# Kernel optimization log

Hardware: AMD Instinct MI355X
Metric: run time of the kernel (lower is better)

The kernel has to match this reference:

```python
import jax, jax.numpy as jnp
import numpy as np

N_NODES = 40000
N_EDGES = 640000
D = 128
D_OUT = 128


def _layernorm(x, gamma, beta, eps=1e-5):
    mu = jnp.mean(x, axis=-1, keepdims=True)
    var = jnp.mean(jnp.square(x - mu), axis=-1, keepdims=True)
    return (x - mu) * jax.lax.rsqrt(var + eps) * gamma + beta


def setup_inputs() -> dict:
    key = jax.random.key(0)
    ks = jax.random.split(key, 6)
    x = jax.random.normal(ks[0], (N_NODES, D), dtype=jnp.float32)
    edge_index = jax.random.randint(ks[1], (2, N_EDGES), 0, N_NODES, dtype=jnp.int64)
    s = 1.0 / np.sqrt(D)
    return {
        "x": x,
        "edge_index": edge_index,
        "ln1_w": jnp.ones((D,), jnp.float32),
        "ln1_b": jnp.zeros((D,), jnp.float32),
        "ln2_w": jnp.ones((D,), jnp.float32),
        "ln2_b": jnp.zeros((D,), jnp.float32),
        "w": jnp.ones((D,), jnp.float32),
        "W1": jax.random.normal(ks[2], (D, D), jnp.float32) * s,
        "W2": jax.random.normal(ks[3], (D, D), jnp.float32) * s,
        "O1": jax.random.normal(ks[4], (2 * D, D), jnp.float32) * s,
        "O2": jax.random.normal(ks[5], (D, D_OUT), jnp.float32) * s,
    }


def reference(x, edge_index, ln1_w, ln1_b, ln2_w, ln2_b, w, W1, W2, O1, O2):
    row, col = edge_index[0], edge_index[1]
    n = x.shape[0]
    # gather + 2-layer message MLP (bias-free): [E, D]
    msg = jnp.maximum(x[row] @ W1, 0.0) @ W2
    # scatter_mean over destination nodes (zero where no incoming edges)
    agg = jax.ops.segment_sum(msg, col, num_segments=n)
    cnt = jax.ops.segment_sum(jnp.ones((msg.shape[0],), x.dtype), col, num_segments=n)
    agg = agg / jnp.maximum(cnt, 1.0)[:, None]
    agg_n = _layernorm(agg, ln1_w, ln1_b)
    # repulsion + residual + LayerNorm
    fx = _layernorm(x + (x - agg_n) * w, ln2_w, ln2_b)
    # concat + output MLP
    cat = jnp.concatenate([fx, agg_n], axis=1)
    return jnp.maximum(cat @ O1, 0.0) @ O2
```

## Files before the change

### kernel.cpp

```cpp
#include <hip/hip_runtime.h>
#include <hip/hip_bf16.h>

#define NN 40000
#define NE 640000
#define DD 128
#define CAP 64
#define SLICE 5000
#define FILLB 640
#define FCHUNK 8000

typedef __attribute__((ext_vector_type(8))) short bf16x8;
typedef __attribute__((ext_vector_type(8))) unsigned short u16x8;
typedef __attribute__((ext_vector_type(4))) float f32x4;

__device__ __forceinline__ unsigned short f2bf(float f) {
    __hip_bfloat16 h = __float2bfloat16(f);
    return *reinterpret_cast<unsigned short*>(&h);
}
__device__ __forceinline__ float bf2f(unsigned short u) {
    union { unsigned int ui; float f; } v;
    v.ui = ((unsigned int)u) << 16;
    return v.f;
}

__global__ __launch_bounds__(256) void prep_kernel(
    const float* __restrict__ W1, const float* __restrict__ W2,
    const float* __restrict__ O1, const float* __restrict__ O2,
    unsigned short* __restrict__ w1t, unsigned short* __restrict__ w2t,
    unsigned short* __restrict__ o1t, unsigned short* __restrict__ o2t,
    unsigned int* __restrict__ cnt)
{
    int bx = blockIdx.x;
    if (bx >= 320) {
        int t = (bx - 320) * 256 + threadIdx.x;
        if (t < NN) cnt[t] = 0u;
        return;
    }
    int t = bx * 256 + threadIdx.x;
    if (t < 16384) {
        int n = t >> 7, k = t & 127;
        w1t[t] = f2bf(W1[k * 128 + n]);
    } else if (t < 32768) {
        int i = t - 16384;
        int n = i >> 7, k = i & 127;
        w2t[i] = f2bf(W2[k * 128 + n]);
    } else if (t < 65536) {
        int i = t - 32768;
        int n = i >> 8, k = i & 255;
        o1t[i] = f2bf(O1[k * 128 + n]);
    } else {
        int i = t - 65536;
        int n = i >> 7, k = i & 127;
        o2t[i] = f2bf(O2[k * 128 + n]);
    }
}

__global__ __launch_bounds__(256) void mega1_kernel(
    const float* __restrict__ x, const unsigned short* __restrict__ w1t,
    const unsigned short* __restrict__ w2t, unsigned short* __restrict__ nm,
    const int* __restrict__ ei, unsigned int* __restrict__ cnt,
    unsigned short* __restrict__ srcs)
{
    __shared__ unsigned short xt[64 * 128];
    __shared__ unsigned short wb[128 * 128];
    const int tid = threadIdx.x;
    const int bx = blockIdx.x;

    if (bx >= 625) {
        const int fb = bx - 625;
        const int slice = bx & 7;
        const int rank = fb >> 3;
        const int base = rank * FCHUNK;
        for (int j = tid; j < FCHUNK; j += 256) {
            int e = base + j;
            int d = ei[NE + e];
            int s = ei[e];
            if ((unsigned)d / SLICE == (unsigned)slice) {
                unsigned int p = atomicAdd(cnt + d, 1u);
                if (p < CAP) srcs[(size_t)d * CAP + p] = (unsigned short)s;
            }
        }
        return;
    }

    const int row0 = bx * 64;

    #pragma unroll
    for (int it = 0; it < 4; ++it) {
        int c = tid + it * 256;
        int r = c >> 4;
        int c0 = (c & 15) << 3;
        const float4* gp = reinterpret_cast<const float4*>(x + (size_t)(row0 + r) * DD + c0);
        float4 f0 = gp[0], f1 = gp[1];
        u16x8 p;
        p[0] = f2bf(f0.x); p[1] = f2bf(f0.y); p[2] = f2bf(f0.z); p[3] = f2bf(f0.w);
        p[4] = f2bf(f1.x); p[5] = f2bf(f1.y); p[6] = f2bf(f1.z); p[7] = f2bf(f1.w);
        unsigned b = (unsigned)((r * DD + c0) * 2) ^ ((unsigned)(r & 7) << 4);
        *reinterpret_cast<u16x8*>(reinterpret_cast<char*>(xt) + b) = p;
    }
    #pragma unroll
    for (int it = 0; it < 8; ++it) {
        int c = tid + it * 256;
        int n = c >> 4;
        int k0 = (c & 15) << 3;
        u16x8 v = *reinterpret_cast<const u16x8*>(w1t + n * DD + k0);
        unsigned b = (unsigned)((n * DD + k0) * 2) ^ ((unsigned)(n & 7) << 4);
        *reinterpret_cast<u16x8*>(reinterpret_cast<char*>(wb) + b) = v;
    }
    __syncthreads();

    const int lane = tid & 63;
    const int wv = tid >> 6;
    const int l15 = lane & 15;
    const int lg = lane >> 4;

    f32x4 acc[8];
    #pragma unroll
    for (int i = 0; i < 8; ++i) acc[i] = (f32x4){0.f, 0.f, 0.f, 0.f};

    #pragma unroll
    for (int kk = 0; kk < 4; ++kk) {
        int k = kk * 32 + lg * 8;
        int ar = wv * 16 + l15;
        bf16x8 a = *reinterpret_cast<const bf16x8*>(
            reinterpret_cast<const char*>(xt) + ((unsigned)((ar * DD + k) * 2) ^ ((unsigned)(ar & 7) << 4)));
        #pragma unroll
        for (int n0 = 0; n0 < 8; ++n0) {
            int bn = n0 * 16 + l15;
            bf16x8 bf = *reinterpret_cast<const bf16x8*>(
                reinterpret_cast<const char*>(wb) + ((unsigned)((bn * DD + k) * 2) ^ ((unsigned)(bn & 7) << 4)));
            acc[n0] = __builtin_amdgcn_mfma_f32_16x16x32_bf16(a, bf, acc[n0], 0, 0, 0);
        }
    }
    __syncthreads();

    unsigned short* hb = xt;
    #pragma unroll
    for (int n0 = 0; n0 < 8; ++n0) {
        #pragma unroll
        for (int ri = 0; ri < 4; ++ri) {
            int r = wv * 16 + lg * 4 + ri;
            int cc = n0 * 16 + l15;
            float v = fmaxf(acc[n0][ri], 0.0f);
            *reinterpret_cast<unsigned short*>(
                reinterpret_cast<char*>(hb) + ((unsigned)((r * DD + cc) * 2) ^ ((unsigned)(r & 7) << 4))) = f2bf(v);
        }
    }
    #pragma unroll
    for (int it = 0; it < 8; ++it) {
        int c = tid + it * 256;
        int n = c >> 4;
        int k0 = (c & 15) << 3;
        u16x8 v = *reinterpret_cast<const u16x8*>(w2t + n * DD + k0);
        unsigned b = (unsigned)((n * DD + k0) * 2) ^ ((unsigned)(n & 7) << 4);
        *reinterpret_cast<u16x8*>(reinterpret_cast<char*>(wb) + b) = v;
    }
    __syncthreads();

    f32x4 acc2[8];
    #pragma unroll
    for (int i = 0; i < 8; ++i) acc2[i] = (f32x4){0.f, 0.f, 0.f, 0.f};
    #pragma unroll
    for (int kk = 0; kk < 4; ++kk) {
        int k = kk * 32 + lg * 8;
        int ar = wv * 16 + l15;
        bf16x8 a = *reinterpret_cast<const bf16x8*>(
            reinterpret_cast<const char*>(hb) + ((unsigned)((ar * DD + k) * 2) ^ ((unsigned)(ar & 7) << 4)));
        #pragma unroll
        for (int n0 = 0; n0 < 8; ++n0) {
            int bn = n0 * 16 + l15;
            bf16x8 bf = *reinterpret_cast<const bf16x8*>(
                reinterpret_cast<const char*>(wb) + ((unsigned)((bn * DD + k) * 2) ^ ((unsigned)(bn & 7) << 4)));
            acc2[n0] = __builtin_amdgcn_mfma_f32_16x16x32_bf16(a, bf, acc2[n0], 0, 0, 0);
        }
    }
    #pragma unroll
    for (int n0 = 0; n0 < 8; ++n0) {
        #pragma unroll
        for (int ri = 0; ri < 4; ++ri) {
            int r = row0 + wv * 16 + lg * 4 + ri;
            int cc = n0 * 16 + l15;
            nm[(size_t)r * DD + cc] = f2bf(acc2[n0][ri]);
        }
    }
}

__global__ __launch_bounds__(256) void pull_node_kernel(
    const unsigned short* __restrict__ nm, const unsigned short* __restrict__ srcs,
    const unsigned int* __restrict__ cnt,
    const float* __restrict__ x,
    const float* __restrict__ g1, const float* __restrict__ b1,
    const float* __restrict__ g2, const float* __restrict__ b2,
    const float* __restrict__ w, unsigned short* __restrict__ catb)
{
    const int lane = threadIdx.x & 63;
    const int wv = threadIdx.x >> 6;
    const int i = blockIdx.x * 4 + wv;
    const int d0 = lane * 2;

    const unsigned int degf = cnt[i];
    const int deg = (int)(degf < CAP ? degf : CAP);
    const unsigned short* sp = srcs + (size_t)i * CAP;

    float a0 = 0.f, a1 = 0.f;
    int e = 0;
    for (; e + 8 <= deg; e += 8) {
        int s[8];
        #pragma unroll
        for (int j = 0; j < 8; ++j) s[j] = sp[e + j];
        ushort2 m[8];
        #pragma unroll
        for (int j = 0; j < 8; ++j)
            m[j] = *reinterpret_cast<const ushort2*>(nm + (size_t)s[j] * DD + d0);
        #pragma unroll
        for (int j = 0; j < 8; ++j) { a0 += bf2f(m[j].x); a1 += bf2f(m[j].y); }
    }
    for (; e + 4 <= deg; e += 4) {
        int s0 = sp[e + 0], s1 = sp[e + 1], s2 = sp[e + 2], s3 = sp[e + 3];
        ushort2 m0 = *reinterpret_cast<const ushort2*>(nm + (size_t)s0 * DD + d0);
        ushort2 m1 = *reinterpret_cast<const ushort2*>(nm + (size_t)s1 * DD + d0);
        ushort2 m2 = *reinterpret_cast<const ushort2*>(nm + (size_t)s2 * DD + d0);
        ushort2 m3 = *reinterpret_cast<const ushort2*>(nm + (size_t)s3 * DD + d0);
        a0 += bf2f(m0.x) + bf2f(m1.x) + bf2f(m2.x) + bf2f(m3.x);
        a1 += bf2f(m0.y) + bf2f(m1.y) + bf2f(m2.y) + bf2f(m3.y);
    }
    for (; e < deg; ++e) {
        int s0 = sp[e];
        ushort2 m0 = *reinterpret_cast<const ushort2*>(nm + (size_t)s0 * DD + d0);
        a0 += bf2f(m0.x);
        a1 += bf2f(m0.y);
    }

    float inv = 1.0f / fmaxf((float)degf, 1.0f);
    a0 *= inv; a1 *= inv;

    float s = a0 + a1;
    #pragma unroll
    for (int o = 32; o > 0; o >>= 1) s += __shfl_xor(s, o, 64);
    float mu = s * (1.0f / 128.0f);
    float e0 = a0 - mu, e1 = a1 - mu;
    float q = e0 * e0 + e1 * e1;
    #pragma unroll
    for (int o = 32; o > 0; o >>= 1) q += __shfl_xor(q, o, 64);
    float rs = rsqrtf(q * (1.0f / 128.0f) + 1e-5f);

    float2 g1v = *reinterpret_cast<const float2*>(g1 + d0);
    float2 b1v = *reinterpret_cast<const float2*>(b1 + d0);
    float an0 = e0 * rs * g1v.x + b1v.x;
    float an1 = e1 * rs * g1v.y + b1v.y;

    float2 xv = *reinterpret_cast<const float2*>(x + (size_t)i * DD + d0);
    float2 wv2 = *reinterpret_cast<const float2*>(w + d0);
    float t0 = xv.x + (xv.x - an0) * wv2.x;
    float t1 = xv.y + (xv.y - an1) * wv2.y;

    float s2 = t0 + t1;
    #pragma unroll
    for (int o = 32; o > 0; o >>= 1) s2 += __shfl_xor(s2, o, 64);
    float mu2 = s2 * (1.0f / 128.0f);
    float f0 = t0 - mu2, f1 = t1 - mu2;
    float q2 = f0 * f0 + f1 * f1;
    #pragma unroll
    for (int o = 32; o > 0; o >>= 1) q2 += __shfl_xor(q2, o, 64);
    float rs2 = rsqrtf(q2 * (1.0f / 128.0f) + 1e-5f);

    float2 g2v = *reinterpret_cast<const float2*>(g2 + d0);
    float2 b2v = *reinterpret_cast<const float2*>(b2 + d0);
    float fx0 = f0 * rs2 * g2v.x + b2v.x;
    float fx1 = f1 * rs2 * g2v.y + b2v.y;

    ushort2 uo; uo.x = f2bf(fx0); uo.y = f2bf(fx1);
    *reinterpret_cast<ushort2*>(catb + (size_t)i * 256 + d0) = uo;
    ushort2 ua; ua.x = f2bf(an0); ua.y = f2bf(an1);
    *reinterpret_cast<ushort2*>(catb + (size_t)i * 256 + 128 + d0) = ua;
}

__global__ __launch_bounds__(256) void mlp2_kernel(
    const unsigned short* __restrict__ catb, const unsigned short* __restrict__ o1t,
    const unsigned short* __restrict__ o2t, float* __restrict__ out)
{
    __shared__ unsigned short ct[64 * 128];
    __shared__ unsigned short wb[128 * 128];
    const int tid = threadIdx.x;
    const int row0 = blockIdx.x * 64;
    const int lane = tid & 63;
    const int wv = tid >> 6;
    const int l15 = lane & 15;
    const int lg = lane >> 4;

    f32x4 acc[8];
    #pragma unroll
    for (int i = 0; i < 8; ++i) acc[i] = (f32x4){0.f, 0.f, 0.f, 0.f};

    for (int h = 0; h < 2; ++h) {
        #pragma unroll
        for (int it = 0; it < 4; ++it) {
            int c = tid + it * 256;
            int r = c >> 4;
            int c0 = (c & 15) << 3;
            u16x8 v = *reinterpret_cast<const u16x8*>(catb + (size_t)(row0 + r) * 256 + h * 128 + c0);
            unsigned b = (unsigned)((r * 128 + c0) * 2) ^ ((unsigned)(r & 7) << 4);
            *reinterpret_cast<u16x8*>(reinterpret_cast<char*>(ct) + b) = v;
        }
        #pragma unroll
        for (int it = 0; it < 8; ++it) {
            int c = tid + it * 256;
            int n = c >> 4;
            int k0 = (c & 15) << 3;
            u16x8 v = *reinterpret_cast<const u16x8*>(o1t + n * 256 + h * 128 + k0);
            unsigned b = (unsigned)((n * 128 + k0) * 2) ^ ((unsigned)(n & 7) << 4);
            *reinterpret_cast<u16x8*>(reinterpret_cast<char*>(wb) + b) = v;
        }
        __syncthreads();
        #pragma unroll
        for (int kk = 0; kk < 4; ++kk) {
            int k = kk * 32 + lg * 8;
            int ar = wv * 16 + l15;
            bf16x8 a = *reinterpret_cast<const bf16x8*>(
                reinterpret_cast<const char*>(ct) + ((unsigned)((ar * 128 + k) * 2) ^ ((unsigned)(ar & 7) << 4)));
            #pragma unroll
            for (int n0 = 0; n0 < 8; ++n0) {
                int bn = n0 * 16 + l15;
                bf16x8 bf = *reinterpret_cast<const bf16x8*>(
                    reinterpret_cast<const char*>(wb) + ((unsigned)((bn * 128 + k) * 2) ^ ((unsigned)(bn & 7) << 4)));
                acc[n0] = __builtin_amdgcn_mfma_f32_16x16x32_bf16(a, bf, acc[n0], 0, 0, 0);
            }
        }
        __syncthreads();
    }

    unsigned short* hb = ct;
    #pragma unroll
    for (int n0 = 0; n0 < 8; ++n0) {
        #pragma unroll
        for (int ri = 0; ri < 4; ++ri) {
            int r = wv * 16 + lg * 4 + ri;
            int cc = n0 * 16 + l15;
            float v = fmaxf(acc[n0][ri], 0.0f);
            *reinterpret_cast<unsigned short*>(
                reinterpret_cast<char*>(hb) + ((unsigned)((r * DD + cc) * 2) ^ ((unsigned)(r & 7) << 4))) = f2bf(v);
        }
    }
    #pragma unroll
    for (int it = 0; it < 8; ++it) {
        int c = tid + it * 256;
        int n = c >> 4;
        int k0 = (c & 15) << 3;
        u16x8 v = *reinterpret_cast<const u16x8*>(o2t + n * DD + k0);
        unsigned b = (unsigned)((n * DD + k0) * 2) ^ ((unsigned)(n & 7) << 4);
        *reinterpret_cast<u16x8*>(reinterpret_cast<char*>(wb) + b) = v;
    }
    __syncthreads();

    f32x4 acc2[8];
    #pragma unroll
    for (int i = 0; i < 8; ++i) acc2[i] = (f32x4){0.f, 0.f, 0.f, 0.f};
    #pragma unroll
    for (int kk = 0; kk < 4; ++kk) {
        int k = kk * 32 + lg * 8;
        int ar = wv * 16 + l15;
        bf16x8 a = *reinterpret_cast<const bf16x8*>(
            reinterpret_cast<const char*>(hb) + ((unsigned)((ar * DD + k) * 2) ^ ((unsigned)(ar & 7) << 4)));
        #pragma unroll
        for (int n0 = 0; n0 < 8; ++n0) {
            int bn = n0 * 16 + l15;
            bf16x8 bf = *reinterpret_cast<const bf16x8*>(
                reinterpret_cast<const char*>(wb) + ((unsigned)((bn * DD + k) * 2) ^ ((unsigned)(bn & 7) << 4)));
            acc2[n0] = __builtin_amdgcn_mfma_f32_16x16x32_bf16(a, bf, acc2[n0], 0, 0, 0);
        }
    }

    #pragma unroll
    for (int n0 = 0; n0 < 8; ++n0) {
        #pragma unroll
        for (int ri = 0; ri < 4; ++ri) {
            int r = row0 + wv * 16 + lg * 4 + ri;
            int cc = n0 * 16 + l15;
            out[(size_t)r * DD + cc] = acc2[n0][ri];
        }
    }
}

extern "C" void kernel_launch(void* const* d_in, const int* in_sizes, int n_in,
                              void* d_out, int out_size, void* d_ws, size_t ws_size,
                              hipStream_t stream) {
    const float* x   = (const float*)d_in[0];
    const int*   ei  = (const int*)d_in[1];
    const float* g1  = (const float*)d_in[2];
    const float* b1  = (const float*)d_in[3];
    const float* g2  = (const float*)d_in[4];
    const float* b2  = (const float*)d_in[5];
    const float* w   = (const float*)d_in[6];
    const float* W1  = (const float*)d_in[7];
    const float* W2  = (const float*)d_in[8];
    const float* O1  = (const float*)d_in[9];
    const float* O2  = (const float*)d_in[10];
    float* out = (float*)d_out;

    char* ws = (char*)d_ws;
    unsigned short* nm   = (unsigned short*)(ws);
    unsigned short* catb = (unsigned short*)(ws + 10240000);
    unsigned short* srcs = (unsigned short*)(ws + 30720000);
    unsigned int*   cnt  = (unsigned int*)(ws + 35840000);
    unsigned short* w1t  = (unsigned short*)(ws + 36000000);
    unsigned short* w2t  = (unsigned short*)(ws + 36032768);
    unsigned short* o1t  = (unsigned short*)(ws + 36065536);
    unsigned short* o2t  = (unsigned short*)(ws + 36131072);

    prep_kernel<<<477, 256, 0, stream>>>(W1, W2, O1, O2, w1t, w2t, o1t, o2t, cnt);
    mega1_kernel<<<625 + FILLB, 256, 0, stream>>>(x, w1t, w2t, nm, ei, cnt, srcs);
    pull_node_kernel<<<NN / 4, 256, 0, stream>>>(nm, srcs, cnt, x, g1, b1, g2, b2, w, catb);
    mlp2_kernel<<<NN / 64, 256, 0, stream>>>(catb, o1t, o2t, out);
}
```

Before: 175.3 us.

## Pre-swizzle weights and load them directly to LDS; simplify edge fill

The prep kernel now writes transposed bf16 weights in the XOR-swizzled LDS layout, so the GEMM kernels can copy them with global_load_lds DMA without going through registers. The weight loads are issued before the activation staging and the previous epilogue so they overlap. The edge-bucketing fill blocks drop the 8-way slice filtering and use 250 blocks that each handle 10 edges per thread with batched loads, atomics and nontemporal stores. This removes redundant edge reads, but the atomics are no longer grouped by destination slice and may contend more.

```diff
diff --git a/kernel.cpp b/kernel.cpp
--- a/kernel.cpp
+++ b/kernel.cpp
@@ -5,9 +5,7 @@
 #define NE 640000
 #define DD 128
 #define CAP 64
-#define SLICE 5000
-#define FILLB 640
-#define FCHUNK 8000
+#define FILLB 250
 
 typedef __attribute__((ext_vector_type(8))) short bf16x8;
 typedef __attribute__((ext_vector_type(8))) unsigned short u16x8;
@@ -21,6 +19,11 @@
     union { unsigned int ui; float f; } v;
     v.ui = ((unsigned int)u) << 16;
     return v.f;
+}
+__device__ __forceinline__ void gload16(void* lds, const void* g) {
+    __builtin_amdgcn_global_load_lds(
+        (const __attribute__((address_space(1))) void*)g,
+        (__attribute__((address_space(3))) void*)lds, 16, 0, 0);
 }
 
 __global__ __launch_bounds__(256) void prep_kernel(
@@ -39,19 +42,24 @@
     int t = bx * 256 + threadIdx.x;
     if (t < 16384) {
         int n = t >> 7, k = t & 127;
-        w1t[t] = f2bf(W1[k * 128 + n]);
+        unsigned b = (unsigned)(n * 256) + (((unsigned)(k * 2)) ^ (((unsigned)(n & 7)) << 4));
+        w1t[b >> 1] = f2bf(W1[k * 128 + n]);
     } else if (t < 32768) {
         int i = t - 16384;
         int n = i >> 7, k = i & 127;
-        w2t[i] = f2bf(W2[k * 128 + n]);
+        unsigned b = (unsigned)(n * 256) + (((unsigned)(k * 2)) ^ (((unsigned)(n & 7)) << 4));
+        w2t[b >> 1] = f2bf(W2[k * 128 + n]);
     } else if (t < 65536) {
         int i = t - 32768;
         int n = i >> 8, k = i & 255;
-        o1t[i] = f2bf(O1[k * 128 + n]);
+        unsigned b = (unsigned)(n * 512 + (k >> 7) * 256)
+                   + (((unsigned)((k & 127) * 2)) ^ (((unsigned)(n & 7)) << 4));
+        o1t[b >> 1] = f2bf(O1[k * 128 + n]);
     } else {
         int i = t - 65536;
         int n = i >> 7, k = i & 127;
-        o2t[i] = f2bf(O2[k * 128 + n]);
+        unsigned b = (unsigned)(n * 256) + (((unsigned)(k * 2)) ^ (((unsigned)(n & 7)) << 4));
+        o2t[b >> 1] = f2bf(O2[k * 128 + n]);
     }
 }
 
@@ -67,24 +75,32 @@
     const int bx = blockIdx.x;
 
     if (bx >= 625) {
-        const int fb = bx - 625;
-        const int slice = bx & 7;
-        const int rank = fb >> 3;
-        const int base = rank * FCHUNK;
-        for (int j = tid; j < FCHUNK; j += 256) {
-            int e = base + j;
-            int d = ei[NE + e];
-            int s = ei[e];
-            if ((unsigned)d / SLICE == (unsigned)slice) {
-                unsigned int p = atomicAdd(cnt + d, 1u);
-                if (p < CAP) srcs[(size_t)d * CAP + p] = (unsigned short)s;
-            }
-        }
+        const int base = (bx - 625) * 2560 + tid;
+        int s[10], d[10];
+        #pragma unroll
+        for (int j = 0; j < 10; ++j) d[j] = ei[NE + base + j * 256];
+        #pragma unroll
+        for (int j = 0; j < 10; ++j) s[j] = ei[base + j * 256];
+        unsigned int p[10];
+        #pragma unroll
+        for (int j = 0; j < 10; ++j) p[j] = atomicAdd(cnt + d[j], 1u);
+        #pragma unroll
+        for (int j = 0; j < 10; ++j)
+            if (p[j] < CAP)
+                __builtin_nontemporal_store((unsigned short)s[j],
+                                            srcs + (size_t)d[j] * CAP + p[j]);
         return;
     }
 
     const int row0 = bx * 64;
-
+    const int lane = tid & 63;
+    const int wv = tid >> 6;
+
+    #pragma unroll
+    for (int it = 0; it < 8; ++it) {
+        int b = (wv * 8 + it) * 1024;
+        gload16((char*)wb + b, (const char*)w1t + b + lane * 16);
+    }
     #pragma unroll
     for (int it = 0; it < 4; ++it) {
         int c = tid + it * 256;
@@ -98,19 +114,8 @@
         unsigned b = (unsigned)((r * DD + c0) * 2) ^ ((unsigned)(r & 7) << 4);
         *reinterpret_cast<u16x8*>(reinterpret_cast<char*>(xt) + b) = p;
     }
-    #pragma unroll
-    for (int it = 0; it < 8; ++it) {
-        int c = tid + it * 256;
-        int n = c >> 4;
-        int k0 = (c & 15) << 3;
-        u16x8 v = *reinterpret_cast<const u16x8*>(w1t + n * DD + k0);
-        unsigned b = (unsigned)((n * DD + k0) * 2) ^ ((unsigned)(n & 7) << 4);
-        *reinterpret_cast<u16x8*>(reinterpret_cast<char*>(wb) + b) = v;
-    }
     __syncthreads();
 
-    const int lane = tid & 63;
-    const int wv = tid >> 6;
     const int l15 = lane & 15;
     const int lg = lane >> 4;
 
@@ -134,6 +139,11 @@
     }
     __syncthreads();
 
+    #pragma unroll
+    for (int it = 0; it < 8; ++it) {
+        int b = (wv * 8 + it) * 1024;
+        gload16((char*)wb + b, (const char*)w2t + b + lane * 16);
+    }
     unsigned short* hb = xt;
     #pragma unroll
     for (int n0 = 0; n0 < 8; ++n0) {
@@ -145,15 +155,6 @@
             *reinterpret_cast<unsigned short*>(
                 reinterpret_cast<char*>(hb) + ((unsigned)((r * DD + cc) * 2) ^ ((unsigned)(r & 7) << 4))) = f2bf(v);
         }
-    }
-    #pragma unroll
-    for (int it = 0; it < 8; ++it) {
-        int c = tid + it * 256;
-        int n = c >> 4;
-        int k0 = (c & 15) << 3;
-        u16x8 v = *reinterpret_cast<const u16x8*>(w2t + n * DD + k0);
-        unsigned b = (unsigned)((n * DD + k0) * 2) ^ ((unsigned)(n & 7) << 4);
-        *reinterpret_cast<u16x8*>(reinterpret_cast<char*>(wb) + b) = v;
     }
     __syncthreads();
 
@@ -294,6 +295,13 @@
 
     for (int h = 0; h < 2; ++h) {
         #pragma unroll
+        for (int it = 0; it < 8; ++it) {
+            int Lb = (wv * 8 + it) * 1024;
+            int n = (Lb >> 8) + (lane >> 4);
+            int c2 = (lane & 15) * 16;
+            gload16((char*)wb + Lb, (const char*)o1t + n * 512 + h * 256 + c2);
+        }
+        #pragma unroll
         for (int it = 0; it < 4; ++it) {
             int c = tid + it * 256;
             int r = c >> 4;
@@ -301,15 +309,6 @@
             u16x8 v = *reinterpret_cast<const u16x8*>(catb + (size_t)(row0 + r) * 256 + h * 128 + c0);
             unsigned b = (unsigned)((r * 128 + c0) * 2) ^ ((unsigned)(r & 7) << 4);
             *reinterpret_cast<u16x8*>(reinterpret_cast<char*>(ct) + b) = v;
-        }
-        #pragma unroll
-        for (int it = 0; it < 8; ++it) {
-            int c = tid + it * 256;
-            int n = c >> 4;
-            int k0 = (c & 15) << 3;
-            u16x8 v = *reinterpret_cast<const u16x8*>(o1t + n * 256 + h * 128 + k0);
-            unsigned b = (unsigned)((n * 128 + k0) * 2) ^ ((unsigned)(n & 7) << 4);
-            *reinterpret_cast<u16x8*>(reinterpret_cast<char*>(wb) + b) = v;
         }
         __syncthreads();
         #pragma unroll
@@ -329,6 +328,11 @@
         __syncthreads();
     }
 
+    #pragma unroll
+    for (int it = 0; it < 8; ++it) {
+        int b = (wv * 8 + it) * 1024;
+        gload16((char*)wb + b, (const char*)o2t + b + lane * 16);
+    }
     unsigned short* hb = ct;
     #pragma unroll
     for (int n0 = 0; n0 < 8; ++n0) {
@@ -340,15 +344,6 @@
             *reinterpret_cast<unsigned short*>(
                 reinterpret_cast<char*>(hb) + ((unsigned)((r * DD + cc) * 2) ^ ((unsigned)(r & 7) << 4))) = f2bf(v);
         }
-    }
-    #pragma unroll
-    for (int it = 0; it < 8; ++it) {
-        int c = tid + it * 256;
-        int n = c >> 4;
-        int k0 = (c & 15) << 3;
-        u16x8 v = *reinterpret_cast<const u16x8*>(o2t + n * DD + k0);
-        unsigned b = (unsigned)((n * DD + k0) * 2) ^ ((unsigned)(n & 7) << 4);
-        *reinterpret_cast<u16x8*>(reinterpret_cast<char*>(wb) + b) = v;
     }
     __syncthreads();
 
```

New measurement: 178.3 us. No clear change (+1.7%).
